# Optimization experiments

Hardware: AMD Instinct MI355X
Metric: run time of the kernel (lower is better)

Reference implementation:

```python
import jax, jax.numpy as jnp
from jax import lax
import numpy as np

FS = 48000
N_CHANNELS = 40
LOW_FREQ = 50
BATCH = 8
T_SAMPLES = 96000  # 2 s at 48 kHz
DOWN_FACTOR = 24   # 48 kHz -> 2 kHz envelope rate


def make_erb_fcoefs(fs, n_channels, low_freq):
    """Port of make_ERB_filters (Slaney gammatone coefficients). (C, 10)."""
    T = 1.0 / fs
    EarQ, minBW = 9.26449, 24.7
    i = np.arange(1, n_channels + 1, dtype=np.float64)
    hi = fs / 2
    cf = -(EarQ * minBW) + np.exp(i * (-np.log(hi + EarQ * minBW) + np.log(low_freq + EarQ * minBW)) / n_channels) * (hi + EarQ * minBW)
    erb = cf / EarQ + minBW
    B = 1.019 * 2 * np.pi * erb
    c = np.cos(2 * cf * np.pi * T)
    s = np.sin(2 * cf * np.pi * T)
    e = np.exp(B * T)
    sp = np.sqrt(3 + 2 ** 1.5)
    sm = np.sqrt(3 - 2 ** 1.5)
    a0 = T
    b1 = -2 * c / e
    b2 = np.exp(-2 * B * T)
    a11 = -(2 * T * c / e + 2 * sp * T * s / e) / 2
    a12 = -(2 * T * c / e - 2 * sp * T * s / e) / 2
    a13 = -(2 * T * c / e + 2 * sm * T * s / e) / 2
    a14 = -(2 * T * c / e - 2 * sm * T * s / e) / 2
    z = np.exp(4j * cf * np.pi * T)
    w = np.exp(-(B * T) + 2j * cf * np.pi * T)
    gain = np.abs(
        (-2 * z * T + 2 * w * T * (c - sm * s)) *
        (-2 * z * T + 2 * w * T * (c + sm * s)) *
        (-2 * z * T + 2 * w * T * (c - sp * s)) *
        (-2 * z * T + 2 * w * T * (c + sp * s)) /
        (-2 / np.exp(2 * B * T) - 2 * z + 2 * (1 + z) / np.exp(B * T)) ** 4)
    fcoefs = np.stack([np.full_like(cf, a0), a11, a12, a13, a14,
                       np.zeros_like(cf), np.ones_like(cf), b1, b2, gain], axis=1)
    return fcoefs.astype(np.float32)


def setup_inputs() -> dict:
    key = jax.random.key(0)
    x = jax.random.normal(key, (BATCH, T_SAMPLES), dtype=jnp.float32)
    fcoefs = jnp.asarray(make_erb_fcoefs(FS, N_CHANNELS, LOW_FREQ))
    return {"x": x, "fcoefs": fcoefs}


def _erb_filter_bank(x, fcoefs):
    """Cascaded 4-stage biquad gammatone bank. x: (B, T) -> (B, C, T)."""
    C = fcoefs.shape[0]
    Bsz = x.shape[0]
    a0 = fcoefs[:, 0]
    a2 = fcoefs[:, 5]  # zeros
    gain = fcoefs[:, 9]
    # numerator coeffs per stage, (4, 3, C); stage 1 divided by gain
    num = jnp.stack([
        jnp.stack([a0 / gain, fcoefs[:, 1] / gain, a2 / gain]),
        jnp.stack([a0, fcoefs[:, 2], a2]),
        jnp.stack([a0, fcoefs[:, 3], a2]),
        jnp.stack([a0, fcoefs[:, 4], a2]),
    ])
    d1 = fcoefs[:, 7]  # denominator (b0 == 1)
    d2 = fcoefs[:, 8]

    def step(carry, xt):
        s1, s2 = carry  # each (4, B, C): DF-II-transposed states per stage
        xk = jnp.broadcast_to(xt[:, None], (Bsz, C))
        ns1, ns2 = [], []
        for k in range(4):
            y = num[k, 0] * xk + s1[k]
            ns1.append(num[k, 1] * xk - d1 * y + s2[k])
            ns2.append(num[k, 2] * xk - d2 * y)
            xk = y
        return (jnp.stack(ns1), jnp.stack(ns2)), xk

    s0 = jnp.zeros((4, Bsz, C), x.dtype)
    _, ys = lax.scan(step, (s0, s0), x.T)  # ys: (T, B, C)
    return jnp.transpose(ys, (1, 2, 0))    # (B, C, T)


def reference(x, fcoefs):
    sub = _erb_filter_bank(x, fcoefs)          # (B, C, T)
    sub = jax.nn.relu(sub)                      # half-wave rectification
    Bsz, C, T = sub.shape
    env = sub.reshape(Bsz, C, T // DOWN_FACTOR, DOWN_FACTOR).mean(-1)  # avg-pool downsample
    return env  # (B, C, T/DOWN_FACTOR)
```

## Files before the change

### kernel.cpp

```cpp
#include <hip/hip_runtime.h>


typedef float f32x2 __attribute__((ext_vector_type(2)));

#define NCH  40
#define NB   8
#define NCP  20
#define TS   96000
#define DOWN 24
#define NSEG 256
#define SEG  375
#define TD   4000
#define NLVL 8
#define INV24 (1.0f/24.0f)

typedef double DMat[4][4][2][2];

__device__ __forceinline__ void dmatcopy(DMat dst, const DMat src) {
    #pragma unroll
    for (int i = 0; i < 4; i++)
        #pragma unroll
        for (int j = 0; j < 4; j++) if (j <= i)
            #pragma unroll
            for (int r = 0; r < 2; r++)
                #pragma unroll
                for (int c = 0; c < 2; c++)
                    dst[i][j][r][c] = src[i][j][r][c];
}

__device__ __forceinline__ void dmatmul(DMat C, const DMat A, const DMat B) {
    #pragma unroll
    for (int i = 0; i < 4; i++)
        #pragma unroll
        for (int j = 0; j < 4; j++) if (j <= i)
            #pragma unroll
            for (int r = 0; r < 2; r++)
                #pragma unroll
                for (int c = 0; c < 2; c++) {
                    double acc = 0.0;
                    #pragma unroll
                    for (int k = 0; k < 4; k++) if (k >= j && k <= i)
                        #pragma unroll
                        for (int q = 0; q < 2; q++)
                            acc += A[i][k][r][q] * B[k][j][q][c];
                    C[i][j][r][c] = acc;
                }
}

__global__ __launch_bounds__(64)
void cochlea_setup(const float* __restrict__ fcoefs, double* __restrict__ ws)
{
    const int c = (int)threadIdx.x;
    if (c >= NCH) return;
    const float* fc = fcoefs + c * 10;
    const double a0  = (double)fc[0];
    const double n11 = (double)fc[2], n12 = (double)fc[3], n13 = (double)fc[4];
    const double nd1 = -(double)fc[7], nd2 = -(double)fc[8];

    double s[8];
    auto step0 = [&]() {
        double y0 = s[0];
        s[0] = nd1 * y0 + s[1];
        s[1] = nd2 * y0;
        double y1 = a0 * y0 + s[2];
        s[2] = nd1 * y1 + (n11 * y0 + s[3]);
        s[3] = nd2 * y1;
        double y2 = a0 * y1 + s[4];
        s[4] = nd1 * y2 + (n12 * y1 + s[5]);
        s[5] = nd2 * y2;
        double y3 = a0 * y2 + s[6];
        s[6] = nd1 * y3 + (n13 * y2 + s[7]);
        s[7] = nd2 * y3;
    };

    DMat A, P, T;
    #pragma unroll
    for (int j = 0; j < 8; j++) {
        #pragma unroll
        for (int i = 0; i < 8; i++) s[i] = (i == j) ? 1.0 : 0.0;
        step0();
        #pragma unroll
        for (int i = 0; i < 8; i++)
            if ((i >> 1) >= (j >> 1))
                A[i >> 1][j >> 1][i & 1][j & 1] = s[i];
    }

    dmatcopy(P, A);
    const int bits[8] = {0, 1, 1, 1, 0, 1, 1, 1};
    #pragma unroll
    for (int t = 0; t < 8; t++) {
        dmatmul(T, P, P);
        if (bits[t]) dmatmul(P, T, A);
        else         dmatcopy(P, T);
    }

    double* o = ws + (size_t)c * (NLVL * 40);
    for (int k = 0; k < NLVL; k++) {
        #pragma unroll
        for (int rb = 0; rb < 4; rb++)
            #pragma unroll
            for (int cb = 0; cb < 4; cb++) if (cb <= rb)
                #pragma unroll
                for (int ri = 0; ri < 2; ri++)
                    #pragma unroll
                    for (int ci = 0; ci < 2; ci++)
                        o[k * 40 + (rb * (rb + 1) / 2 + cb) * 4 + ri * 2 + ci] = P[rb][cb][ri][ci];
        if (k < NLVL - 1) { dmatmul(T, P, P); dmatcopy(P, T); }
    }
}

__global__ __launch_bounds__(256, 1)
void cochlea_main(const float* __restrict__ x,
                  const float* __restrict__ fcoefs,
                  const double* __restrict__ ws,
                  float* __restrict__ out)
{
    const int b  = (int)blockIdx.x;
    const int cp = (int)blockIdx.y;
    const int g  = (int)threadIdx.x;

    const float* fA = fcoefs + cp * 10;
    const float* fB = fcoefs + (cp + NCP) * 10;

    auto mk2 = [](float u, float v) { f32x2 r; r.x = u; r.y = v; return r; };
    const f32x2 va0  = mk2(fA[0], fB[0]);
    const f32x2 vn00 = mk2(fA[0] / fA[9], fB[0] / fB[9]);
    const f32x2 vn10 = mk2(fA[1] / fA[9], fB[1] / fB[9]);
    const f32x2 vn11 = mk2(fA[2], fB[2]);
    const f32x2 vn12 = mk2(fA[3], fB[3]);
    const f32x2 vn13 = mk2(fA[4], fB[4]);
    const f32x2 vnd1 = mk2(-fA[7], -fB[7]);
    const f32x2 vnd2 = mk2(-fA[8], -fB[8]);
    const f32x2 vz   = mk2(0.f, 0.f);

    f32x2 S[8];
    auto stepp = [&](float xu) -> f32x2 {
        f32x2 xv = mk2(xu, xu);
        f32x2 y0 = __builtin_elementwise_fma(vn00, xv, S[0]);
        S[0] = __builtin_elementwise_fma(vnd1, y0, __builtin_elementwise_fma(vn10, xv, S[1]));
        S[1] = vnd2 * y0;
        f32x2 y1 = __builtin_elementwise_fma(va0, y0, S[2]);
        S[2] = __builtin_elementwise_fma(vnd1, y1, __builtin_elementwise_fma(vn11, y0, S[3]));
        S[3] = vnd2 * y1;
        f32x2 y2 = __builtin_elementwise_fma(va0, y1, S[4]);
        S[4] = __builtin_elementwise_fma(vnd1, y2, __builtin_elementwise_fma(vn12, y1, S[5]));
        S[5] = vnd2 * y2;
        f32x2 y3 = __builtin_elementwise_fma(va0, y2, S[6]);
        S[6] = __builtin_elementwise_fma(vnd1, y3, __builtin_elementwise_fma(vn13, y2, S[7]));
        S[7] = vnd2 * y3;
        return y3;
    };

    const float3* xb3 = reinterpret_cast<const float3*>(x + (size_t)b * TS + (size_t)g * SEG);
    float3 bA[5], bB[5];
    auto loadg = [&](float3 (&bf)[5], int m) {
        #pragma unroll
        for (int q = 0; q < 5; q++) bf[q] = xb3[m * 5 + q];
    };

    #pragma unroll
    for (int i = 0; i < 8; i++) S[i] = vz;
    auto c1 = [&](const float3 (&bf)[5]) {
        #pragma unroll
        for (int q = 0; q < 5; q++) { stepp(bf[q].x); stepp(bf[q].y); stepp(bf[q].z); }
    };
    loadg(bA, 0);
    for (int p = 0; p < 12; p++) {
        loadg(bB, 2 * p + 1);
        c1(bA);
        loadg(bA, 2 * p + 2);
        c1(bB);
    }
    c1(bA);

    __shared__ double tk[2][NSEG][9];
    float iA[8], iB[8];

    auto run_scan = [&](const double* wsc, const double (&ei)[8], float (&oi)[8]) {
        int cur = 0;
        #pragma unroll
        for (int i = 0; i < 8; i++) tk[0][g][i] = ei[i];
        __syncthreads();
        double td[8];
        #pragma unroll
        for (int i = 0; i < 8; i++) td[i] = ei[i];
        for (int k = 0; k < NLVL; k++) {
            double M[40];
            #pragma unroll
            for (int q = 0; q < 40; q++) M[q] = wsc[k * 40 + q];
            const int d = 1 << k;
            if (g >= d) {
                double pr[8];
                #pragma unroll
                for (int i = 0; i < 8; i++) pr[i] = tk[cur][g - d][i];
                double nt[8];
                #pragma unroll
                for (int rb = 0; rb < 4; rb++)
                    #pragma unroll
                    for (int ri = 0; ri < 2; ri++) {
                        double acc = td[2 * rb + ri];
                        #pragma unroll
                        for (int cb = 0; cb < 4; cb++) if (cb <= rb)
                            #pragma unroll
                            for (int ci = 0; ci < 2; ci++)
                                acc += M[(rb * (rb + 1) / 2 + cb) * 4 + ri * 2 + ci] * pr[2 * cb + ci];
                        nt[2 * rb + ri] = acc;
                    }
                #pragma unroll
                for (int i = 0; i < 8; i++) td[i] = nt[i];
            }
            #pragma unroll
            for (int i = 0; i < 8; i++) tk[cur ^ 1][g][i] = td[i];
            __syncthreads();
            cur ^= 1;
        }
        #pragma unroll
        for (int i = 0; i < 8; i++) oi[i] = (g == 0) ? 0.f : (float)tk[cur][g - 1][i];
        __syncthreads();
    };

    {
        double e[8];
        #pragma unroll
        for (int i = 0; i < 8; i++) e[i] = (double)S[i].x;
        run_scan(ws + (size_t)cp * (NLVL * 40), e, iA);
        #pragma unroll
        for (int i = 0; i < 8; i++) e[i] = (double)S[i].y;
        run_scan(ws + (size_t)(cp + NCP) * (NLVL * 40), e, iB);
    }

    #pragma unroll
    for (int i = 0; i < 8; i++) S[i] = mk2(iA[i], iB[i]);

    const int g8      = g & 7;
    const int offset  = (15 * g8) % 24;
    const int r       = (24 - offset) % 24;
    const bool hashead = (offset != 0);
    const int hh      = hashead ? 1 : 0;
    const int w0      = (SEG * g + r) / 24;
    const int ph      = (1 + 5 * g8) & 7;
    float* outA = out + ((size_t)b * NCH + cp) * TD;
    float* outB = out + ((size_t)b * NCH + cp + NCP) * TD;

    f32x2 acc = vz, head = vz;
    int kb = 0;

    auto c2 = [&](const float3 (&bf)[5], int m) {
        #pragma unroll
        for (int q = 0; q < 5; q++) {
            float3 v = bf[q];
            acc += __builtin_elementwise_max(stepp(v.x), vz);
            acc += __builtin_elementwise_max(stepp(v.y), vz);
            acc += __builtin_elementwise_max(stepp(v.z), vz);
            int jj = m * 5 + q;
            if (((jj + ph) & 7) == 0) {
                bool ishead = hashead && (kb == 0);
                if (ishead) head = acc;
                else {
                    int idx = w0 + kb - hh;
                    outA[idx] = acc.x * INV24;
                    outB[idx] = acc.y * INV24;
                }
                kb++;
                acc = vz;
            }
        }
    };
    loadg(bA, 0);
    for (int p = 0; p < 12; p++) {
        loadg(bB, 2 * p + 1);
        c2(bA, 2 * p);
        loadg(bA, 2 * p + 2);
        c2(bB, 2 * p + 1);
    }
    c2(bA, 24);

    float hx = __shfl_down(head.x, 1, 64);
    float hy = __shfl_down(head.y, 1, 64);
    if (g8 != 7) {
        int idx = w0 + kb - hh;
        outA[idx] = (acc.x + hx) * INV24;
        outB[idx] = (acc.y + hy) * INV24;
    }
}

extern "C" void kernel_launch(void* const* d_in, const int* in_sizes, int n_in,
                              void* d_out, int out_size, void* d_ws, size_t ws_size,
                              hipStream_t stream) {
    const float* x      = (const float*)d_in[0];
    const float* fcoefs = (const float*)d_in[1];
    float* out = (float*)d_out;
    double* ws = (double*)d_ws;

    cochlea_setup<<<1, 64, 0, stream>>>(fcoefs, ws);
    dim3 grid(NB, NCP);
    cochlea_main<<<grid, 256, 0, stream>>>(x, fcoefs, ws, out);
}
```

Measured before the change: 113.6 us.

## Triple-buffer input loads and stage scan matrices in LDS

The input streaming loops move from double to triple buffering, so each register chunk is loaded two chunks ahead and global load latency is hidden further behind the serial IIR recurrence. The per-level scan matrices are now fetched cooperatively at kernel start and kept in shared memory. This replaces each thread reading 40 doubles from global memory at every scan level. The cost is more registers for the extra buffer and about 5 KB more LDS.

```diff
diff --git a/kernel.cpp b/kernel.cpp
--- a/kernel.cpp
+++ b/kernel.cpp
@@ -118,6 +118,16 @@
     const int b  = (int)blockIdx.x;
     const int cp = (int)blockIdx.y;
     const int g  = (int)threadIdx.x;
+
+    const double* wsA = ws + (size_t)cp * (NLVL * 40);
+    const double* wsB = ws + (size_t)(cp + NCP) * (NLVL * 40);
+    double m0, m1, m2 = 0.0;
+    {
+        int i1 = g + 256;
+        m0 = wsA[g];
+        m1 = (i1 < 320) ? wsA[i1] : wsB[i1 - 320];
+        if (g < 128) m2 = wsB[g + 192];
+    }
 
     const float* fA = fcoefs + cp * 10;
     const float* fB = fcoefs + (cp + NCP) * 10;
@@ -152,7 +162,7 @@
     };
 
     const float3* xb3 = reinterpret_cast<const float3*>(x + (size_t)b * TS + (size_t)g * SEG);
-    float3 bA[5], bB[5];
+    float3 bA[5], bB[5], bC[5];
     auto loadg = [&](float3 (&bf)[5], int m) {
         #pragma unroll
         for (int q = 0; q < 5; q++) bf[q] = xb3[m * 5 + q];
@@ -164,19 +174,26 @@
         #pragma unroll
         for (int q = 0; q < 5; q++) { stepp(bf[q].x); stepp(bf[q].y); stepp(bf[q].z); }
     };
-    loadg(bA, 0);
-    for (int p = 0; p < 12; p++) {
-        loadg(bB, 2 * p + 1);
-        c1(bA);
-        loadg(bA, 2 * p + 2);
-        c1(bB);
-    }
+    loadg(bA, 0); loadg(bB, 1);
+    for (int p = 0; p < 7; p++) {
+        loadg(bC, 3 * p + 2); c1(bA);
+        loadg(bA, 3 * p + 3); c1(bB);
+        loadg(bB, 3 * p + 4); c1(bC);
+    }
+    loadg(bC, 23); c1(bA);
+    loadg(bA, 24); c1(bB);
+    c1(bC);
     c1(bA);
 
+    __shared__ double Mlds[2 * NLVL * 40];
     __shared__ double tk[2][NSEG][9];
+    Mlds[g] = m0;
+    Mlds[g + 256] = m1;
+    if (g < 128) Mlds[g + 512] = m2;
+
     float iA[8], iB[8];
 
-    auto run_scan = [&](const double* wsc, const double (&ei)[8], float (&oi)[8]) {
+    auto run_scan = [&](int ch, const double (&ei)[8], float (&oi)[8]) {
         int cur = 0;
         #pragma unroll
         for (int i = 0; i < 8; i++) tk[0][g][i] = ei[i];
@@ -185,9 +202,7 @@
         #pragma unroll
         for (int i = 0; i < 8; i++) td[i] = ei[i];
         for (int k = 0; k < NLVL; k++) {
-            double M[40];
-            #pragma unroll
-            for (int q = 0; q < 40; q++) M[q] = wsc[k * 40 + q];
+            const double* Mk = &Mlds[ch * 320 + k * 40];
             const int d = 1 << k;
             if (g >= d) {
                 double pr[8];
@@ -203,7 +218,7 @@
                         for (int cb = 0; cb < 4; cb++) if (cb <= rb)
                             #pragma unroll
                             for (int ci = 0; ci < 2; ci++)
-                                acc += M[(rb * (rb + 1) / 2 + cb) * 4 + ri * 2 + ci] * pr[2 * cb + ci];
+                                acc += Mk[(rb * (rb + 1) / 2 + cb) * 4 + ri * 2 + ci] * pr[2 * cb + ci];
                         nt[2 * rb + ri] = acc;
                     }
                 #pragma unroll
@@ -223,10 +238,10 @@
         double e[8];
         #pragma unroll
         for (int i = 0; i < 8; i++) e[i] = (double)S[i].x;
-        run_scan(ws + (size_t)cp * (NLVL * 40), e, iA);
+        run_scan(0, e, iA);
         #pragma unroll
         for (int i = 0; i < 8; i++) e[i] = (double)S[i].y;
-        run_scan(ws + (size_t)(cp + NCP) * (NLVL * 40), e, iB);
+        run_scan(1, e, iB);
     }
 
     #pragma unroll
@@ -266,13 +281,15 @@
             }
         }
     };
-    loadg(bA, 0);
-    for (int p = 0; p < 12; p++) {
-        loadg(bB, 2 * p + 1);
-        c2(bA, 2 * p);
-        loadg(bA, 2 * p + 2);
-        c2(bB, 2 * p + 1);
-    }
+    loadg(bA, 0); loadg(bB, 1);
+    for (int p = 0; p < 7; p++) {
+        loadg(bC, 3 * p + 2); c2(bA, 3 * p);
+        loadg(bA, 3 * p + 3); c2(bB, 3 * p + 1);
+        loadg(bB, 3 * p + 4); c2(bC, 3 * p + 2);
+    }
+    loadg(bC, 23); c2(bA, 21);
+    loadg(bA, 24); c2(bB, 22);
+    c2(bC, 23);
     c2(bA, 24);
 
     float hx = __shfl_down(head.x, 1, 64);
```

Result: no change. 112.2 us (-1.2%).
